# Optimization experiments

Measured on AMD Instinct MI355X. Metric: run time of the kernel, lower is better.

## Reference

```python
import jax, jax.numpy as jnp
import numpy as np

VOCAB, HID, L, HEADS, INTER, MAXSEQ, NCLS = 30522, 128, 2, 2, 512, 512, 2
HEAD = HID // HEADS
B, S = 128, 512


def _tlin(x, W, b):
    # TernaryLinear: threshold-quantize W to {-1,0,1} with per-tensor scale,
    # then ordinary linear. delta = 0.7*mean|W|, alpha = mean|W| over kept entries.
    absW = jnp.abs(W)
    delta = 0.7 * jnp.mean(absW)
    mask = (absW > delta).astype(W.dtype)
    alpha = jnp.sum(absW * mask) / jnp.maximum(jnp.sum(mask), 1.0)
    Wq = jnp.sign(W) * mask * alpha  # [out, in]
    return jnp.einsum('...i,oi->...o', x, Wq) + b


def _ln(x, g, b, eps=1e-5):
    m = jnp.mean(x, axis=-1, keepdims=True)
    v = jnp.var(x, axis=-1, keepdims=True)
    return (x - m) * jax.lax.rsqrt(v + eps) * g + b


def setup_inputs() -> dict:
    key = jax.random.key(0)
    ks = iter(jax.random.split(key, 64))
    n = lambda shape, s=0.02: jax.random.normal(next(ks), shape, dtype=jnp.float32) * s
    inp = {
        'input_ids': jax.random.randint(next(ks), (B, S), 0, VOCAB, dtype=jnp.int32).astype(jnp.int64),
        'tok_emb': n((VOCAB, HID)),
        'pos_emb': n((MAXSEQ, HID)),
        'ln_g': jnp.ones((HID,), jnp.float32), 'ln_b': jnp.zeros((HID,), jnp.float32),
        'qw': n((L, HID, HID)), 'qb': jnp.zeros((L, HID), jnp.float32),
        'kw': n((L, HID, HID)), 'kb': jnp.zeros((L, HID), jnp.float32),
        'vw': n((L, HID, HID)), 'vb': jnp.zeros((L, HID), jnp.float32),
        'aow': n((L, HID, HID)), 'aob': jnp.zeros((L, HID), jnp.float32),
        'iw': n((L, INTER, HID)), 'ib': jnp.zeros((L, INTER), jnp.float32),
        'fow': n((L, HID, INTER)), 'fob': jnp.zeros((L, HID), jnp.float32),
        'ln1g': jnp.ones((L, HID), jnp.float32), 'ln1b': jnp.zeros((L, HID), jnp.float32),
        'ln2g': jnp.ones((L, HID), jnp.float32), 'ln2b': jnp.zeros((L, HID), jnp.float32),
        'clf_w': n((NCLS, HID)), 'clf_b': jnp.zeros((NCLS,), jnp.float32),
    }
    return inp


def reference(input_ids, tok_emb, pos_emb, ln_g, ln_b, qw, qb, kw, kb, vw, vb,
              aow, aob, iw, ib, fow, fob, ln1g, ln1b, ln2g, ln2b, clf_w, clf_b):
    b, s = input_ids.shape
    x = tok_emb[input_ids] + pos_emb[jnp.arange(s)][None, :, :]  # [B,S,H]
    x = _ln(x, ln_g, ln_b)
    scale = 1.0 / (HEAD ** 0.5)
    for l in range(L):
        q = _tlin(x, qw[l], qb[l]).reshape(b, s, HEADS, HEAD)
        k = _tlin(x, kw[l], kb[l]).reshape(b, s, HEADS, HEAD)
        v = _tlin(x, vw[l], vb[l]).reshape(b, s, HEADS, HEAD)
        scores = jnp.einsum('bqhd,bkhd->bhqk', q, k) * scale
        attn = jax.nn.softmax(scores, axis=-1)
        ctx = jnp.einsum('bhqk,bkhd->bqhd', attn, v).reshape(b, s, HID)
        attn_out = _tlin(ctx, aow[l], aob[l])
        x = _ln(x + attn_out, ln1g[l], ln1b[l])
        ff = _tlin(jax.nn.relu(_tlin(x, iw[l], ib[l])), fow[l], fob[l])
        x = _ln(x + ff, ln2g[l], ln2b[l])
    cls = x[:, 0, :]
    logits = _tlin(cls, clf_w, clf_b)  # [B, NCLS]
    return logits
```

## Files before the change

### kernel.cpp

```cpp
#include <hip/hip_runtime.h>

typedef short bf8s __attribute__((ext_vector_type(8)));
typedef float f32x4 __attribute__((ext_vector_type(4)));

#define MFMA16(a, b, c) __builtin_amdgcn_mfma_f32_16x16x32_bf16(a, b, c, 0, 0, 0)

constexpr int S_ = 512, HID_ = 128, B_ = 128, M_ = B_ * S_;

__device__ inline short f2bf(float f) {
  unsigned u = __float_as_uint(f);
  u = (u + 0x7fffu + ((u >> 16) & 1u)) >> 16;
  return (short)u;
}
__device__ inline float bf2f(short s) {
  return __uint_as_float(((unsigned)(unsigned short)s) << 16);
}

__device__ inline float block_red1024(float v, float* red) {
  #pragma unroll
  for (int m = 32; m >= 1; m >>= 1) v += __shfl_xor(v, m);
  __syncthreads();
  if ((threadIdx.x & 63) == 0) red[threadIdx.x >> 6] = v;
  __syncthreads();
  float t = 0.f;
  #pragma unroll
  for (int i = 0; i < 16; ++i) t += red[i];
  return t;
}

__device__ inline void mat_info(int mat, const float* qw, const float* kw,
                                const float* vw, const float* aow, const float* iw,
                                const float* fw, const float* cw,
                                const float** src, int* n, int* doff) {
  if (mat < 6) {
    int l = mat / 3, which = mat % 3;
    const float* t[3] = {qw, kw, vw};
    *src = t[which] + l * 16384; *n = 16384; *doff = l * 49152 + which * 16384;
  } else if (mat < 8) {
    int l = mat - 6;
    *src = aow + l * 16384; *n = 16384; *doff = 98304 + l * 16384;
  } else if (mat < 10) {
    *src = iw + (mat - 8) * 65536; *n = 65536; *doff = 131072 + (mat - 8) * 65536;
  } else if (mat < 12) {
    *src = fw + (mat - 10) * 65536; *n = 65536; *doff = 262144 + (mat - 10) * 65536;
  } else {
    *src = cw; *n = 256; *doff = 393216;
  }
}

__global__ __launch_bounds__(1024) void k_qe(const float* qw, const float* kw,
    const float* vw, const float* aow, const float* iw, const float* fw,
    const float* cw, short* WQ,
    const int* __restrict__ ids, const float* __restrict__ tok,
    const float* __restrict__ pos, const float* __restrict__ g,
    const float* __restrict__ bb, short* xb) {
  __shared__ float red[16];
  int tid = threadIdx.x;
  if (blockIdx.x < 13) {
    const float* src; int n, doff;
    mat_info(blockIdx.x, qw, kw, vw, aow, iw, fw, cw, &src, &n, &doff);
    float s = 0.f;
    for (int i = tid; i < n; i += 1024) s += fabsf(src[i]);
    s = block_red1024(s, red);
    float delta = 0.7f * s / (float)n;
    float s2 = 0.f, c2 = 0.f;
    for (int i = tid; i < n; i += 1024) {
      float a = fabsf(src[i]);
      if (a > delta) { s2 += a; c2 += 1.f; }
    }
    s2 = block_red1024(s2, red);
    c2 = block_red1024(c2, red);
    float alpha = s2 / fmaxf(c2, 1.f);
    for (int i = tid; i < n; i += 1024) {
      float w = src[i];
      WQ[doff + i] = (fabsf(w) > delta) ? f2bf(w > 0.f ? alpha : -alpha) : (short)0;
    }
  } else {
    int wave = tid >> 6, lane = tid & 63;
    int t = (blockIdx.x - 13) * 16 + wave;
    int s = t & (S_ - 1);
    int id = ids[t];
    float e0 = tok[(size_t)id * HID_ + lane] + pos[(size_t)s * HID_ + lane];
    float e1 = tok[(size_t)id * HID_ + 64 + lane] + pos[(size_t)s * HID_ + 64 + lane];
    float sum = e0 + e1, ssq = e0 * e0 + e1 * e1;
    #pragma unroll
    for (int m = 32; m >= 1; m >>= 1) {
      sum += __shfl_xor(sum, m);
      ssq += __shfl_xor(ssq, m);
    }
    float mean = sum / 128.f;
    float var = ssq / 128.f - mean * mean;
    float rs = rsqrtf(var + 1e-5f);
    size_t o = (size_t)t * HID_;
    xb[o + lane]      = f2bf((e0 - mean) * rs * g[lane] + bb[lane]);
    xb[o + 64 + lane] = f2bf((e1 - mean) * rs * g[64 + lane] + bb[64 + lane]);
  }
}

__global__ __launch_bounds__(256) void k_qkv(
    const short* __restrict__ A, const short* __restrict__ W,
    const float* __restrict__ b0, const float* __restrict__ b1,
    const float* __restrict__ b2, short* outb) {
  __shared__ short Wl[128 * 144];
  int tid = threadIdx.x, lane = tid & 63, wave = tid >> 6;
  int row16 = lane & 15, quad = lane >> 4;
  int tok0 = blockIdx.x * 64 + wave * 16;
  int nbase = blockIdx.y * 128;

  const short* arow = A + (size_t)(tok0 + row16) * 128 + quad * 8;
  bf8s av[4];
  #pragma unroll
  for (int ki = 0; ki < 4; ++ki) av[ki] = *(const bf8s*)(arow + ki * 32);

  {
    int r = tid >> 1, half = tid & 1;
    const short* src = W + (size_t)(nbase + r) * 128 + half * 64;
    short* dst = &Wl[r * 144 + half * 64];
    #pragma unroll
    for (int j = 0; j < 8; ++j)
      *(bf8s*)(dst + j * 8) = *(const bf8s*)(src + j * 8);
  }
  __syncthreads();

  f32x4 acc[8] = {};
  #pragma unroll
  for (int ki = 0; ki < 4; ++ki)
    #pragma unroll
    for (int ot = 0; ot < 8; ++ot) {
      bf8s b = *(const bf8s*)(&Wl[(ot * 16 + row16) * 144 + ki * 32 + quad * 8]);
      acc[ot] = MFMA16(av[ki], b, acc[ot]);
    }

  const float* bp = (blockIdx.y == 0) ? b0 : ((blockIdx.y == 1) ? b1 : b2);
  float osc = (blockIdx.y == 0) ? 0.125f : 1.0f;
  int m0 = tok0 + quad * 4;
  #pragma unroll
  for (int ot = 0; ot < 8; ++ot) {
    int col = ot * 16 + row16;
    float bi = bp[col];
    #pragma unroll
    for (int r = 0; r < 4; ++r) {
      float v = (acc[ot][r] + bi) * osc;
      outb[(size_t)(m0 + r) * 384 + nbase + col] = f2bf(v);
    }
  }
}

template <int DOQKV>
__global__ __launch_bounds__(512, 2) void k_aoff(
    const short* __restrict__ cb, const short* __restrict__ Wa,
    const float* __restrict__ aob, const float* __restrict__ ln1g,
    const float* __restrict__ ln1b, const short* __restrict__ Wi,
    const short* __restrict__ Wf, const float* __restrict__ ib,
    const float* __restrict__ fb, const float* __restrict__ ln2g,
    const float* __restrict__ ln2b, short* xb,
    const short* __restrict__ Wqkv2, const float* __restrict__ qb2,
    const float* __restrict__ kb2, const float* __restrict__ vb2,
    short* qkvout) {
  __shared__ short SM[29696];
  int tid = threadIdx.x, lane = tid & 63, wave = tid >> 6;
  int row16 = lane & 15, quad = lane >> 4;
  int tok0 = blockIdx.x * 128 + wave * 16;
  int m0 = tok0 + quad * 4;

  const short* arow = cb + (size_t)(tok0 + row16) * 128 + quad * 8;
  bf8s av[4];
  #pragma unroll
  for (int ki = 0; ki < 4; ++ki) av[ki] = *(const bf8s*)(arow + ki * 32);

  {
    int r = tid >> 2, q4 = tid & 3;
    const short* src = Wa + (size_t)r * 128 + q4 * 32;
    short* dst = &SM[r * 144 + q4 * 32];
    #pragma unroll
    for (int j = 0; j < 4; ++j)
      *(bf8s*)(dst + j * 8) = *(const bf8s*)(src + j * 8);
  }
  __syncthreads();

  f32x4 acc[8] = {};
  #pragma unroll
  for (int ki = 0; ki < 4; ++ki)
    #pragma unroll
    for (int ot = 0; ot < 8; ++ot) {
      bf8s b = *(const bf8s*)(&SM[(ot * 16 + row16) * 144 + ki * 32 + quad * 8]);
      acc[ot] = MFMA16(av[ki], b, acc[ot]);
    }

  {
    float sum[4] = {}, ssq[4] = {};
    #pragma unroll
    for (int ot = 0; ot < 8; ++ot) {
      int col = ot * 16 + row16;
      float bi = aob[col];
      #pragma unroll
      for (int r = 0; r < 4; ++r) {
        float v = acc[ot][r] + bi + bf2f(xb[(size_t)(m0 + r) * HID_ + col]);
        acc[ot][r] = v;
        sum[r] += v; ssq[r] += v * v;
      }
    }
    #pragma unroll
    for (int m = 1; m <= 8; m <<= 1)
      #pragma unroll
      for (int r = 0; r < 4; ++r) {
        sum[r] += __shfl_xor(sum[r], m);
        ssq[r] += __shfl_xor(ssq[r], m);
      }
    float mean[4], rstd[4];
    #pragma unroll
    for (int r = 0; r < 4; ++r) {
      mean[r] = sum[r] / 128.f;
      float var = ssq[r] / 128.f - mean[r] * mean[r];
      rstd[r] = rsqrtf(var + 1e-5f);
    }
    #pragma unroll
    for (int ot = 0; ot < 8; ++ot) {
      int col = ot * 16 + row16;
      float gg = ln1g[col], bb2 = ln1b[col];
      #pragma unroll
      for (int r = 0; r < 4; ++r)
        acc[ot][r] = (acc[ot][r] - mean[r]) * rstd[r] * gg + bb2;
    }
  }

  #pragma unroll
  for (int ot = 0; ot < 8; ++ot) {
    int col = ot * 16 + row16;
    #pragma unroll
    for (int r = 0; r < 4; ++r)
      xb[(size_t)(m0 + r) * HID_ + col] = f2bf(acc[ot][r]);
  }

  __syncthreads();
  {
    short* myX = &SM[wave * 2304];
    #pragma unroll
    for (int ot = 0; ot < 8; ++ot)
      #pragma unroll
      for (int r = 0; r < 4; ++r)
        myX[(quad * 4 + r) * 144 + ot * 16 + row16] = f2bf(acc[ot][r]);
    #pragma unroll
    for (int ki = 0; ki < 4; ++ki)
      av[ki] = *(const bf8s*)(myX + row16 * 144 + ki * 32 + quad * 8);
  }

  int rwi = tid >> 3, q8 = tid & 7;
  int rwf = tid >> 2, qf4 = tid & 3;
  short* SWi = SM;
  short* SWf = SM + 9216;
  short* mySt = SM + 19456 + wave * 1280;
  f32x4 acc2[8] = {};
  for (int c = 0; c < 8; ++c) {
    __syncthreads();
    {
      const short* ws1 = Wi + (size_t)(c * 64 + rwi) * HID_ + q8 * 16;
      const short* ws2 = Wf + (size_t)rwf * 512 + c * 64 + qf4 * 16;
      bf8s a0 = *(const bf8s*)(ws1);
      bf8s a1 = *(const bf8s*)(ws1 + 8);
      bf8s b0 = *(const bf8s*)(ws2);
      bf8s b1 = *(const bf8s*)(ws2 + 8);
      short* dwi = SWi + rwi * 144 + q8 * 16;
      short* dwf = SWf + rwf * 80 + qf4 * 16;
      *(bf8s*)(dwi) = a0; *(bf8s*)(dwi + 8) = a1;
      *(bf8s*)(dwf) = b0; *(bf8s*)(dwf + 8) = b1;
    }
    __syncthreads();

    #pragma unroll
    for (int ot = 0; ot < 4; ++ot) {
      f32x4 hacc = {};
      #pragma unroll
      for (int ki = 0; ki < 4; ++ki) {
        bf8s b = *(const bf8s*)(SWi + (ot * 16 + row16) * 144 + ki * 32 + quad * 8);
        hacc = MFMA16(av[ki], b, hacc);
      }
      float bi = ib[c * 64 + ot * 16 + row16];
      #pragma unroll
      for (int r = 0; r < 4; ++r)
        mySt[(quad * 4 + r) * 80 + ot * 16 + row16] =
            f2bf(fmaxf(hacc[r] + bi, 0.f));
    }
    bf8s ha0 = *(const bf8s*)(mySt + row16 * 80 + quad * 8);
    bf8s ha1 = *(const bf8s*)(mySt + row16 * 80 + 32 + quad * 8);
    #pragma unroll
    for (int ot = 0; ot < 8; ++ot) {
      bf8s bA = *(const bf8s*)(SWf + (ot * 16 + row16) * 80 + quad * 8);
      bf8s bB = *(const bf8s*)(SWf + (ot * 16 + row16) * 80 + 32 + quad * 8);
      acc2[ot] = MFMA16(ha0, bA, acc2[ot]);
      acc2[ot] = MFMA16(ha1, bB, acc2[ot]);
    }
  }

  {
    float sum[4] = {}, ssq[4] = {};
    #pragma unroll
    for (int ot = 0; ot < 8; ++ot) {
      int col = ot * 16 + row16;
      float bi = fb[col];
      #pragma unroll
      for (int r = 0; r < 4; ++r) {
        float v = acc2[ot][r] + bi + bf2f(xb[(size_t)(m0 + r) * HID_ + col]);
        acc2[ot][r] = v;
        sum[r] += v; ssq[r] += v * v;
      }
    }
    #pragma unroll
    for (int m = 1; m <= 8; m <<= 1)
      #pragma unroll
      for (int r = 0; r < 4; ++r) {
        sum[r] += __shfl_xor(sum[r], m);
        ssq[r] += __shfl_xor(ssq[r], m);
      }
    float mean[4], rstd[4];
    #pragma unroll
    for (int r = 0; r < 4; ++r) {
      mean[r] = sum[r] / 128.f;
      float var = ssq[r] / 128.f - mean[r] * mean[r];
      rstd[r] = rsqrtf(var + 1e-5f);
    }
    #pragma unroll
    for (int ot = 0; ot < 8; ++ot) {
      int col = ot * 16 + row16;
      float gg = ln2g[col], bb2 = ln2b[col];
      #pragma unroll
      for (int r = 0; r < 4; ++r) {
        float v = (acc2[ot][r] - mean[r]) * rstd[r] * gg + bb2;
        acc2[ot][r] = v;
        xb[(size_t)(m0 + r) * HID_ + col] = f2bf(v);
      }
    }
  }

  if (DOQKV) {
    __syncthreads();
    bf8s av2[4];
    {
      short* myX = &SM[wave * 2304];
      #pragma unroll
      for (int ot = 0; ot < 8; ++ot)
        #pragma unroll
        for (int r = 0; r < 4; ++r)
          myX[(quad * 4 + r) * 144 + ot * 16 + row16] = f2bf(acc2[ot][r]);
      #pragma unroll
      for (int ki = 0; ki < 4; ++ki)
        av2[ki] = *(const bf8s*)(myX + row16 * 144 + ki * 32 + quad * 8);
    }
    for (int c3 = 0; c3 < 3; ++c3) {
      __syncthreads();
      {
        int r = tid >> 2, q4 = tid & 3;
        const short* src = Wqkv2 + (size_t)(c3 * 128 + r) * 128 + q4 * 32;
        short* dst = &SM[r * 144 + q4 * 32];
        #pragma unroll
        for (int j = 0; j < 4; ++j)
          *(bf8s*)(dst + j * 8) = *(const bf8s*)(src + j * 8);
      }
      __syncthreads();
      f32x4 acc3[8] = {};
      #pragma unroll
      for (int ki = 0; ki < 4; ++ki)
        #pragma unroll
        for (int ot = 0; ot < 8; ++ot) {
          bf8s b = *(const bf8s*)(&SM[(ot * 16 + row16) * 144 + ki * 32 + quad * 8]);
          acc3[ot] = MFMA16(av2[ki], b, acc3[ot]);
        }
      const float* bp = (c3 == 0) ? qb2 : ((c3 == 1) ? kb2 : vb2);
      float osc = (c3 == 0) ? 0.125f : 1.0f;
      #pragma unroll
      for (int ot = 0; ot < 8; ++ot) {
        int col = ot * 16 + row16;
        float bi = bp[col];
        #pragma unroll
        for (int r = 0; r < 4; ++r) {
          float v = (acc3[ot][r] + bi) * osc;
          qkvout[(size_t)(m0 + r) * 384 + c3 * 128 + col] = f2bf(v);
        }
      }
    }
  }
}

__global__ __launch_bounds__(512) void k_attn(const short* __restrict__ qkv,
                                              short* __restrict__ O) {
  __shared__ short Kl[64 * 72];
  __shared__ short Vtl[64 * 72];
  __shared__ short Pl[8][16 * 72];

  int tid = threadIdx.x, lane = tid & 63, wave = tid >> 6;
  int row16 = lane & 15, quad = lane >> 4;
  int b = blockIdx.x >> 2, h = (blockIdx.x >> 1) & 1, qhalf = blockIdx.x & 1;
  const short* base  = qkv + (size_t)b * S_ * 384;
  const short* kbase = base + 128 + h * 64;
  const short* vbase = base + 256 + h * 64;
  int q0 = qhalf * 256 + wave * 32;

  bf8s qa[2][2];
  #pragma unroll
  for (int qf = 0; qf < 2; ++qf) {
    const short* qrow = base + h * 64 +
        (size_t)(q0 + qf * 16 + row16) * 384 + quad * 8;
    qa[qf][0] = *(const bf8s*)(qrow);
    qa[qf][1] = *(const bf8s*)(qrow + 32);
  }

  int krow = tid >> 3, dgk = tid & 7;
  int vkey = tid & 63, dgv = tid >> 6;
  const short* kptr = kbase + (size_t)krow * 384 + dgk * 8;
  const short* vptr = vbase + (size_t)vkey * 384 + dgv * 8;
  bf8s kst = *(const bf8s*)(kptr);
  bf8s vst = *(const bf8s*)(vptr);

  float li[2][4] = {};
  f32x4 oacc[2][4] = {};
  short* myP = &Pl[wave][0];

  for (int kt0 = 0; kt0 < S_; kt0 += 64) {
    if (kt0) __syncthreads();
    *(bf8s*)(&Kl[krow * 72 + dgk * 8]) = kst;
    #pragma unroll
    for (int j = 0; j < 8; ++j) Vtl[(dgv * 8 + j) * 72 + vkey] = vst[j];
    __syncthreads();
    if (kt0 + 64 < S_) {
      kst = *(const bf8s*)(kptr + (size_t)(kt0 + 64) * 384);
      vst = *(const bf8s*)(vptr + (size_t)(kt0 + 64) * 384);
    }

    f32x4 sc[2][4] = {};
    #pragma unroll
    for (int ks = 0; ks < 4; ++ks) {
      const short* kp = &Kl[(ks * 16 + row16) * 72 + quad * 8];
      bf8s k0 = *(const bf8s*)(kp);
      bf8s k1 = *(const bf8s*)(kp + 32);
      sc[0][ks] = MFMA16(qa[0][0], k0, sc[0][ks]);
      sc[0][ks] = MFMA16(qa[0][1], k1, sc[0][ks]);
      sc[1][ks] = MFMA16(qa[1][0], k0, sc[1][ks]);
      sc[1][ks] = MFMA16(qa[1][1], k1, sc[1][ks]);
    }

    #pragma unroll
    for (int qf = 0; qf < 2; ++qf) {
      #pragma unroll
      for (int ks = 0; ks < 4; ++ks)
        #pragma unroll
        for (int r = 0; r < 4; ++r) {
          float pv = __expf(sc[qf][ks][r]);
          li[qf][r] += pv;
          myP[(quad * 4 + r) * 72 + ks * 16 + row16] = f2bf(pv);
        }
      bf8s pa0 = *(const bf8s*)(&myP[row16 * 72 + quad * 8]);
      bf8s pa1 = *(const bf8s*)(&myP[row16 * 72 + 32 + quad * 8]);
      #pragma unroll
      for (int dt = 0; dt < 4; ++dt) {
        const short* vp = &Vtl[(dt * 16 + row16) * 72 + quad * 8];
        bf8s v0 = *(const bf8s*)(vp);
        bf8s v1 = *(const bf8s*)(vp + 32);
        oacc[qf][dt] = MFMA16(pa0, v0, oacc[qf][dt]);
        oacc[qf][dt] = MFMA16(pa1, v1, oacc[qf][dt]);
      }
    }
  }

  #pragma unroll
  for (int qf = 0; qf < 2; ++qf) {
    float inv[4];
    #pragma unroll
    for (int r = 0; r < 4; ++r) {
      float t = li[qf][r];
      #pragma unroll
      for (int m = 1; m <= 8; m <<= 1) t += __shfl_xor(t, m);
      inv[r] = 1.f / t;
    }
    size_t trow = (size_t)(b * S_ + q0 + qf * 16 + quad * 4);
    #pragma unroll
    for (int dt = 0; dt < 4; ++dt)
      #pragma unroll
      for (int r = 0; r < 4; ++r)
        O[(trow + r) * HID_ + h * 64 + dt * 16 + row16] =
            f2bf(oacc[qf][dt][r] * inv[r]);
  }
}

__global__ __launch_bounds__(256) void k_clf(const short* __restrict__ xb,
    const short* __restrict__ Wc, const float* __restrict__ cbias, float* out) {
  int i = threadIdx.x;
  int b = i >> 1, c = i & 1;
  float s = 0.f;
  for (int k = 0; k < HID_; ++k)
    s += bf2f(xb[(size_t)b * S_ * HID_ + k]) * bf2f(Wc[c * HID_ + k]);
  out[b * 2 + c] = s + cbias[c];
}

extern "C" void kernel_launch(void* const* d_in, const int* in_sizes, int n_in,
                              void* d_out, int out_size, void* d_ws, size_t ws_size,
                              hipStream_t stream) {
  const int*   ids     = (const int*)d_in[0];
  const float* tok_emb = (const float*)d_in[1];
  const float* pos_emb = (const float*)d_in[2];
  const float* ln_g    = (const float*)d_in[3];
  const float* ln_bb   = (const float*)d_in[4];
  const float* qw      = (const float*)d_in[5];
  const float* qbias   = (const float*)d_in[6];
  const float* kw      = (const float*)d_in[7];
  const float* kbias   = (const float*)d_in[8];
  const float* vw      = (const float*)d_in[9];
  const float* vbias   = (const float*)d_in[10];
  const float* aow     = (const float*)d_in[11];
  const float* aobias  = (const float*)d_in[12];
  const float* iw      = (const float*)d_in[13];
  const float* ibias   = (const float*)d_in[14];
  const float* fow     = (const float*)d_in[15];
  const float* fbias   = (const float*)d_in[16];
  const float* ln1g    = (const float*)d_in[17];
  const float* ln1b    = (const float*)d_in[18];
  const float* ln2g    = (const float*)d_in[19];
  const float* ln2b    = (const float*)d_in[20];
  const float* clfw    = (const float*)d_in[21];
  const float* clfb    = (const float*)d_in[22];

  char* ws = (char*)d_ws;
  short* WQ  = (short*)ws;
  short* xb  = (short*)(ws + 1048576);
  short* qkv = (short*)(ws + 1048576 + 16777216);
  short* cb_ = qkv + (size_t)M_ * 384;

  k_qe<<<13 + M_ / 16, 1024, 0, stream>>>(qw, kw, vw, aow, iw, fow, clfw, WQ,
                                          ids, tok_emb, pos_emb, ln_g, ln_bb, xb);

  const short* Wqkv0 = WQ;
  const short* Wqkv1 = WQ + 49152;
  const short* Wa0   = WQ + 98304;
  const short* Wa1   = WQ + 98304 + 16384;
  const short* Wi0   = WQ + 131072;
  const short* Wi1   = WQ + 131072 + 65536;
  const short* Wf0   = WQ + 262144;
  const short* Wf1   = WQ + 262144 + 65536;

  k_qkv<<<dim3(M_ / 64, 3), 256, 0, stream>>>(
      xb, Wqkv0, qbias, kbias, vbias, qkv);
  k_attn<<<512, 512, 0, stream>>>(qkv, cb_);
  k_aoff<1><<<M_ / 128, 512, 0, stream>>>(
      cb_, Wa0, aobias, ln1g, ln1b, Wi0, Wf0, ibias, fbias, ln2g, ln2b, xb,
      Wqkv1, qbias + HID_, kbias + HID_, vbias + HID_, qkv);
  k_attn<<<512, 512, 0, stream>>>(qkv, cb_);
  k_aoff<0><<<M_ / 128, 512, 0, stream>>>(
      cb_, Wa1, aobias + HID_, ln1g + HID_, ln1b + HID_, Wi1, Wf1,
      ibias + 512, fbias + HID_, ln2g + HID_, ln2b + HID_, xb,
      nullptr, nullptr, nullptr, nullptr, nullptr);

  k_clf<<<1, 256, 0, stream>>>(xb, WQ + 393216, clfb, (float*)d_out);
}
```

Baseline: 320.0 us.

## Prefetch weight tiles into registers and keep residual in registers in aoff kernel

Register-prefetches the next Wi/Wf chunk and the QKV weight tiles while the current chunk computes, replacing load-then-store staging. Loads the residual early and keeps the LN1 output packed in registers instead of re-reading xb from global memory. Writes the final x through shared memory as coalesced 16-byte rows. Raises the launch-bounds occupancy hint to 4 blocks, which adds register pressure alongside the extra prefetch and residual registers and could cause spills.

Measured after the change: 325.3 us. Within noise of the previous version (+1.7%).

```diff
diff --git a/kernel.cpp b/kernel.cpp
--- a/kernel.cpp
+++ b/kernel.cpp
@@ -147,7 +147,7 @@
 }
 
 template <int DOQKV>
-__global__ __launch_bounds__(512, 2) void k_aoff(
+__global__ __launch_bounds__(512, 4) void k_aoff(
     const short* __restrict__ cb, const short* __restrict__ Wa,
     const float* __restrict__ aob, const float* __restrict__ ln1g,
     const float* __restrict__ ln1b, const short* __restrict__ Wi,
@@ -162,6 +162,8 @@
   int row16 = lane & 15, quad = lane >> 4;
   int tok0 = blockIdx.x * 128 + wave * 16;
   int m0 = tok0 + quad * 4;
+  int rs4 = tid >> 2, q4 = tid & 3;
+  int rwi = tid >> 3, q8 = tid & 7;
 
   const short* arow = cb + (size_t)(tok0 + row16) * 128 + quad * 8;
   bf8s av[4];
@@ -169,13 +171,21 @@
   for (int ki = 0; ki < 4; ++ki) av[ki] = *(const bf8s*)(arow + ki * 32);
 
   {
-    int r = tid >> 2, q4 = tid & 3;
-    const short* src = Wa + (size_t)r * 128 + q4 * 32;
-    short* dst = &SM[r * 144 + q4 * 32];
+    const short* src = Wa + (size_t)rs4 * 128 + q4 * 32;
+    short* dst = &SM[rs4 * 144 + q4 * 32];
     #pragma unroll
     for (int j = 0; j < 4; ++j)
       *(bf8s*)(dst + j * 8) = *(const bf8s*)(src + j * 8);
   }
+
+  float resid[8][4];
+  #pragma unroll
+  for (int ot = 0; ot < 8; ++ot) {
+    int col = ot * 16 + row16;
+    #pragma unroll
+    for (int r = 0; r < 4; ++r)
+      resid[ot][r] = bf2f(xb[(size_t)(m0 + r) * HID_ + col]);
+  }
   __syncthreads();
 
   f32x4 acc[8] = {};
@@ -187,6 +197,14 @@
       acc[ot] = MFMA16(av[ki], b, acc[ot]);
     }
 
+  bf8s pf0, pf1, pf2, pf3;
+  {
+    const short* ws1 = Wi + (size_t)rwi * HID_ + q8 * 16;
+    const short* ws2 = Wf + (size_t)rs4 * 512 + q4 * 16;
+    pf0 = *(const bf8s*)(ws1); pf1 = *(const bf8s*)(ws1 + 8);
+    pf2 = *(const bf8s*)(ws2); pf3 = *(const bf8s*)(ws2 + 8);
+  }
+
   {
     float sum[4] = {}, ssq[4] = {};
     #pragma unroll
@@ -195,7 +213,7 @@
       float bi = aob[col];
       #pragma unroll
       for (int r = 0; r < 4; ++r) {
-        float v = acc[ot][r] + bi + bf2f(xb[(size_t)(m0 + r) * HID_ + col]);
+        float v = acc[ot][r] + bi + resid[ot][r];
         acc[ot][r] = v;
         sum[r] += v; ssq[r] += v * v;
       }
@@ -224,29 +242,31 @@
     }
   }
 
+  unsigned xp[16];
   #pragma unroll
   for (int ot = 0; ot < 8; ++ot) {
-    int col = ot * 16 + row16;
-    #pragma unroll
-    for (int r = 0; r < 4; ++r)
-      xb[(size_t)(m0 + r) * HID_ + col] = f2bf(acc[ot][r]);
+    xp[2 * ot] = (unsigned)(unsigned short)f2bf(acc[ot][0]) |
+                 ((unsigned)(unsigned short)f2bf(acc[ot][1]) << 16);
+    xp[2 * ot + 1] = (unsigned)(unsigned short)f2bf(acc[ot][2]) |
+                     ((unsigned)(unsigned short)f2bf(acc[ot][3]) << 16);
   }
 
   __syncthreads();
-  {
-    short* myX = &SM[wave * 2304];
-    #pragma unroll
-    for (int ot = 0; ot < 8; ++ot)
-      #pragma unroll
-      for (int r = 0; r < 4; ++r)
-        myX[(quad * 4 + r) * 144 + ot * 16 + row16] = f2bf(acc[ot][r]);
+  short* myX = &SM[wave * 2304];
+  {
+    #pragma unroll
+    for (int ot = 0; ot < 8; ++ot) {
+      int col = ot * 16 + row16;
+      myX[(quad * 4 + 0) * 144 + col] = (short)(xp[2 * ot] & 0xffffu);
+      myX[(quad * 4 + 1) * 144 + col] = (short)(xp[2 * ot] >> 16);
+      myX[(quad * 4 + 2) * 144 + col] = (short)(xp[2 * ot + 1] & 0xffffu);
+      myX[(quad * 4 + 3) * 144 + col] = (short)(xp[2 * ot + 1] >> 16);
+    }
     #pragma unroll
     for (int ki = 0; ki < 4; ++ki)
       av[ki] = *(const bf8s*)(myX + row16 * 144 + ki * 32 + quad * 8);
   }
 
-  int rwi = tid >> 3, q8 = tid & 7;
-  int rwf = tid >> 2, qf4 = tid & 3;
   short* SWi = SM;
   short* SWf = SM + 9216;
   short* mySt = SM + 19456 + wave * 1280;
@@ -254,18 +274,22 @@
   for (int c = 0; c < 8; ++c) {
     __syncthreads();
     {
-      const short* ws1 = Wi + (size_t)(c * 64 + rwi) * HID_ + q8 * 16;
-      const short* ws2 = Wf + (size_t)rwf * 512 + c * 64 + qf4 * 16;
-      bf8s a0 = *(const bf8s*)(ws1);
-      bf8s a1 = *(const bf8s*)(ws1 + 8);
-      bf8s b0 = *(const bf8s*)(ws2);
-      bf8s b1 = *(const bf8s*)(ws2 + 8);
       short* dwi = SWi + rwi * 144 + q8 * 16;
-      short* dwf = SWf + rwf * 80 + qf4 * 16;
-      *(bf8s*)(dwi) = a0; *(bf8s*)(dwi + 8) = a1;
-      *(bf8s*)(dwf) = b0; *(bf8s*)(dwf + 8) = b1;
+      short* dwf = SWf + rs4 * 80 + q4 * 16;
+      *(bf8s*)(dwi) = pf0; *(bf8s*)(dwi + 8) = pf1;
+      *(bf8s*)(dwf) = pf2; *(bf8s*)(dwf + 8) = pf3;
     }
     __syncthreads();
+    if (c < 7) {
+      const short* ws1 = Wi + (size_t)((c + 1) * 64 + rwi) * HID_ + q8 * 16;
+      const short* ws2 = Wf + (size_t)rs4 * 512 + (c + 1) * 64 + q4 * 16;
+      pf0 = *(const bf8s*)(ws1); pf1 = *(const bf8s*)(ws1 + 8);
+      pf2 = *(const bf8s*)(ws2); pf3 = *(const bf8s*)(ws2 + 8);
+    } else if (DOQKV) {
+      const short* src = Wqkv2 + (size_t)rs4 * 128 + q4 * 32;
+      pf0 = *(const bf8s*)(src);      pf1 = *(const bf8s*)(src + 8);
+      pf2 = *(const bf8s*)(src + 16); pf3 = *(const bf8s*)(src + 24);
+    }
 
     #pragma unroll
     for (int ot = 0; ot < 4; ++ot) {
@@ -300,7 +324,10 @@
       float bi = fb[col];
       #pragma unroll
       for (int r = 0; r < 4; ++r) {
-        float v = acc2[ot][r] + bi + bf2f(xb[(size_t)(m0 + r) * HID_ + col]);
+        unsigned u = xp[2 * ot + (r >> 1)];
+        float xv = (r & 1) ? __uint_as_float(u & 0xffff0000u)
+                           : __uint_as_float(u << 16);
+        float v = acc2[ot][r] + bi + xv;
         acc2[ot][r] = v;
         sum[r] += v; ssq[r] += v * v;
       }
@@ -324,39 +351,45 @@
       int col = ot * 16 + row16;
       float gg = ln2g[col], bb2 = ln2b[col];
       #pragma unroll
-      for (int r = 0; r < 4; ++r) {
-        float v = (acc2[ot][r] - mean[r]) * rstd[r] * gg + bb2;
-        acc2[ot][r] = v;
-        xb[(size_t)(m0 + r) * HID_ + col] = f2bf(v);
-      }
-    }
+      for (int r = 0; r < 4; ++r)
+        acc2[ot][r] = (acc2[ot][r] - mean[r]) * rstd[r] * gg + bb2;
+    }
+  }
+
+  __syncthreads();
+  #pragma unroll
+  for (int ot = 0; ot < 8; ++ot) {
+    int col = ot * 16 + row16;
+    #pragma unroll
+    for (int r = 0; r < 4; ++r)
+      myX[(quad * 4 + r) * 144 + col] = f2bf(acc2[ot][r]);
+  }
+  {
+    int xr = lane >> 2, xs = (lane & 3) * 32;
+    short* xrow = xb + (size_t)(tok0 + xr) * HID_ + xs;
+    #pragma unroll
+    for (int j = 0; j < 4; ++j)
+      *(bf8s*)(xrow + j * 8) = *(const bf8s*)(myX + xr * 144 + xs + j * 8);
   }
 
   if (DOQKV) {
-    __syncthreads();
     bf8s av2[4];
-    {
-      short* myX = &SM[wave * 2304];
-      #pragma unroll
-      for (int ot = 0; ot < 8; ++ot)
-        #pragma unroll
-        for (int r = 0; r < 4; ++r)
-          myX[(quad * 4 + r) * 144 + ot * 16 + row16] = f2bf(acc2[ot][r]);
-      #pragma unroll
-      for (int ki = 0; ki < 4; ++ki)
-        av2[ki] = *(const bf8s*)(myX + row16 * 144 + ki * 32 + quad * 8);
-    }
+    #pragma unroll
+    for (int ki = 0; ki < 4; ++ki)
+      av2[ki] = *(const bf8s*)(myX + row16 * 144 + ki * 32 + quad * 8);
     for (int c3 = 0; c3 < 3; ++c3) {
       __syncthreads();
       {
-        int r = tid >> 2, q4 = tid & 3;
-        const short* src = Wqkv2 + (size_t)(c3 * 128 + r) * 128 + q4 * 32;
-        short* dst = &SM[r * 144 + q4 * 32];
-        #pragma unroll
-        for (int j = 0; j < 4; ++j)
-          *(bf8s*)(dst + j * 8) = *(const bf8s*)(src + j * 8);
+        short* dst = &SM[rs4 * 144 + q4 * 32];
+        *(bf8s*)(dst) = pf0;      *(bf8s*)(dst + 8) = pf1;
+        *(bf8s*)(dst + 16) = pf2; *(bf8s*)(dst + 24) = pf3;
       }
       __syncthreads();
+      if (c3 < 2) {
+        const short* src = Wqkv2 + (size_t)((c3 + 1) * 128 + rs4) * 128 + q4 * 32;
+        pf0 = *(const bf8s*)(src);      pf1 = *(const bf8s*)(src + 8);
+        pf2 = *(const bf8s*)(src + 16); pf3 = *(const bf8s*)(src + 24);
+      }
       f32x4 acc3[8] = {};
       #pragma unroll
       for (int ki = 0; ki < 4; ++ki)
```

## Read fused-layer weights directly from global memory and drop block barriers

Applied to the files above, without the earlier changes.

Restructures the fused attention-output/FFN kernel so that each wave reads weight fragments straight from global memory (L1/L2-cached) instead of staging them cooperatively in LDS with __syncthreads. Blocks shrink to 256 threads with a small per-wave LDS tile. That tile is used to stage the residual input and to write activations and qkv outputs as coalesced 16-byte rows instead of scattered 2-byte stores. The aim is to remove barrier stalls and LDS capacity limits on occupancy. The cost is more global/L2 weight traffic per wave, since the weights are no longer shared across waves through LDS.

After: 601.6 us. +88.0%, slower.

```diff
diff --git a/kernel.cpp b/kernel.cpp
--- a/kernel.cpp
+++ b/kernel.cpp
@@ -147,7 +147,7 @@
 }
 
 template <int DOQKV>
-__global__ __launch_bounds__(512, 2) void k_aoff(
+__global__ __launch_bounds__(256) void k_aoff(
     const short* __restrict__ cb, const short* __restrict__ Wa,
     const float* __restrict__ aob, const float* __restrict__ ln1g,
     const float* __restrict__ ln1b, const short* __restrict__ Wi,
@@ -157,33 +157,36 @@
     const short* __restrict__ Wqkv2, const float* __restrict__ qb2,
     const float* __restrict__ kb2, const float* __restrict__ vb2,
     short* qkvout) {
-  __shared__ short SM[29696];
+  __shared__ short SM[4 * 2304];
   int tid = threadIdx.x, lane = tid & 63, wave = tid >> 6;
   int row16 = lane & 15, quad = lane >> 4;
-  int tok0 = blockIdx.x * 128 + wave * 16;
+  int tok0 = blockIdx.x * 64 + wave * 16;
   int m0 = tok0 + quad * 4;
+  short* myX = &SM[wave * 2304];
+  int xr = lane >> 2, xs = (lane & 3) * 32;
+
+  {
+    const short* src = xb + (size_t)(tok0 + xr) * HID_ + xs;
+    bf8s x0 = *(const bf8s*)(src);
+    bf8s x1 = *(const bf8s*)(src + 8);
+    bf8s x2 = *(const bf8s*)(src + 16);
+    bf8s x3 = *(const bf8s*)(src + 24);
+    short* dst = myX + xr * 144 + xs;
+    *(bf8s*)(dst) = x0;      *(bf8s*)(dst + 8) = x1;
+    *(bf8s*)(dst + 16) = x2; *(bf8s*)(dst + 24) = x3;
+  }
 
   const short* arow = cb + (size_t)(tok0 + row16) * 128 + quad * 8;
   bf8s av[4];
   #pragma unroll
   for (int ki = 0; ki < 4; ++ki) av[ki] = *(const bf8s*)(arow + ki * 32);
 
-  {
-    int r = tid >> 2, q4 = tid & 3;
-    const short* src = Wa + (size_t)r * 128 + q4 * 32;
-    short* dst = &SM[r * 144 + q4 * 32];
-    #pragma unroll
-    for (int j = 0; j < 4; ++j)
-      *(bf8s*)(dst + j * 8) = *(const bf8s*)(src + j * 8);
-  }
-  __syncthreads();
-
   f32x4 acc[8] = {};
   #pragma unroll
   for (int ki = 0; ki < 4; ++ki)
     #pragma unroll
     for (int ot = 0; ot < 8; ++ot) {
-      bf8s b = *(const bf8s*)(&SM[(ot * 16 + row16) * 144 + ki * 32 + quad * 8]);
+      bf8s b = *(const bf8s*)(Wa + (size_t)(ot * 16 + row16) * 128 + ki * 32 + quad * 8);
       acc[ot] = MFMA16(av[ki], b, acc[ot]);
     }
 
@@ -195,7 +198,7 @@
       float bi = aob[col];
       #pragma unroll
       for (int r = 0; r < 4; ++r) {
-        float v = acc[ot][r] + bi + bf2f(xb[(size_t)(m0 + r) * HID_ + col]);
+        float v = acc[ot][r] + bi + bf2f(myX[(quad * 4 + r) * 144 + col]);
         acc[ot][r] = v;
         sum[r] += v; ssq[r] += v * v;
       }
@@ -229,67 +232,62 @@
     int col = ot * 16 + row16;
     #pragma unroll
     for (int r = 0; r < 4; ++r)
-      xb[(size_t)(m0 + r) * HID_ + col] = f2bf(acc[ot][r]);
-  }
-
-  __syncthreads();
-  {
-    short* myX = &SM[wave * 2304];
-    #pragma unroll
-    for (int ot = 0; ot < 8; ++ot)
-      #pragma unroll
-      for (int r = 0; r < 4; ++r)
-        myX[(quad * 4 + r) * 144 + ot * 16 + row16] = f2bf(acc[ot][r]);
-    #pragma unroll
-    for (int ki = 0; ki < 4; ++ki)
-      av[ki] = *(const bf8s*)(myX + row16 * 144 + ki * 32 + quad * 8);
-  }
-
-  int rwi = tid >> 3, q8 = tid & 7;
-  int rwf = tid >> 2, qf4 = tid & 3;
-  short* SWi = SM;
-  short* SWf = SM + 9216;
-  short* mySt = SM + 19456 + wave * 1280;
+      myX[(quad * 4 + r) * 144 + col] = f2bf(acc[ot][r]);
+  }
+  #pragma unroll
+  for (int ki = 0; ki < 4; ++ki)
+    av[ki] = *(const bf8s*)(myX + row16 * 144 + ki * 32 + quad * 8);
+  {
+    const short* src = myX + xr * 144 + xs;
+    short* dst = xb + (size_t)(tok0 + xr) * HID_ + xs;
+    #pragma unroll
+    for (int j = 0; j < 4; ++j)
+      *(bf8s*)(dst + j * 8) = *(const bf8s*)(src + j * 8);
+  }
+
   f32x4 acc2[8] = {};
   for (int c = 0; c < 8; ++c) {
-    __syncthreads();
-    {
-      const short* ws1 = Wi + (size_t)(c * 64 + rwi) * HID_ + q8 * 16;
-      const short* ws2 = Wf + (size_t)rwf * 512 + c * 64 + qf4 * 16;
-      bf8s a0 = *(const bf8s*)(ws1);
-      bf8s a1 = *(const bf8s*)(ws1 + 8);
-      bf8s b0 = *(const bf8s*)(ws2);
-      bf8s b1 = *(const bf8s*)(ws2 + 8);
-      short* dwi = SWi + rwi * 144 + q8 * 16;
-      short* dwf = SWf + rwf * 80 + qf4 * 16;
-      *(bf8s*)(dwi) = a0; *(bf8s*)(dwi + 8) = a1;
-      *(bf8s*)(dwf) = b0; *(bf8s*)(dwf + 8) = b1;
-    }
-    __syncthreads();
-
     #pragma unroll
     for (int ot = 0; ot < 4; ++ot) {
       f32x4 hacc = {};
       #pragma unroll
       for (int ki = 0; ki < 4; ++ki) {
-        bf8s b = *(const bf8s*)(SWi + (ot * 16 + row16) * 144 + ki * 32 + quad * 8);
+        bf8s b = *(const bf8s*)(Wi + (size_t)(c * 64 + ot * 16 + row16) * 128 + ki * 32 + quad * 8);
         hacc = MFMA16(av[ki], b, hacc);
       }
       float bi = ib[c * 64 + ot * 16 + row16];
       #pragma unroll
       for (int r = 0; r < 4; ++r)
-        mySt[(quad * 4 + r) * 80 + ot * 16 + row16] =
+        myX[(quad * 4 + r) * 80 + ot * 16 + row16] =
             f2bf(fmaxf(hacc[r] + bi, 0.f));
     }
-    bf8s ha0 = *(const bf8s*)(mySt + row16 * 80 + quad * 8);
-    bf8s ha1 = *(const bf8s*)(mySt + row16 * 80 + 32 + quad * 8);
-    #pragma unroll
-    for (int ot = 0; ot < 8; ++ot) {
-      bf8s bA = *(const bf8s*)(SWf + (ot * 16 + row16) * 80 + quad * 8);
-      bf8s bB = *(const bf8s*)(SWf + (ot * 16 + row16) * 80 + 32 + quad * 8);
-      acc2[ot] = MFMA16(ha0, bA, acc2[ot]);
-      acc2[ot] = MFMA16(ha1, bB, acc2[ot]);
-    }
+    {
+      bf8s ha0 = *(const bf8s*)(myX + row16 * 80 + quad * 8);
+      #pragma unroll
+      for (int ot = 0; ot < 8; ++ot) {
+        bf8s bA = *(const bf8s*)(Wf + (size_t)(ot * 16 + row16) * 512 + c * 64 + quad * 8);
+        acc2[ot] = MFMA16(ha0, bA, acc2[ot]);
+      }
+    }
+    {
+      bf8s ha1 = *(const bf8s*)(myX + row16 * 80 + 32 + quad * 8);
+      #pragma unroll
+      for (int ot = 0; ot < 8; ++ot) {
+        bf8s bB = *(const bf8s*)(Wf + (size_t)(ot * 16 + row16) * 512 + c * 64 + 32 + quad * 8);
+        acc2[ot] = MFMA16(ha1, bB, acc2[ot]);
+      }
+    }
+  }
+
+  {
+    const short* src = xb + (size_t)(tok0 + xr) * HID_ + xs;
+    bf8s x0 = *(const bf8s*)(src);
+    bf8s x1 = *(const bf8s*)(src + 8);
+    bf8s x2 = *(const bf8s*)(src + 16);
+    bf8s x3 = *(const bf8s*)(src + 24);
+    short* dst = myX + xr * 144 + xs;
+    *(bf8s*)(dst) = x0;      *(bf8s*)(dst + 8) = x1;
+    *(bf8s*)(dst + 16) = x2; *(bf8s*)(dst + 24) = x3;
   }
 
   {
@@ -300,7 +298,7 @@
       float bi = fb[col];
       #pragma unroll
       for (int r = 0; r < 4; ++r) {
-        float v = acc2[ot][r] + bi + bf2f(xb[(size_t)(m0 + r) * HID_ + col]);
+        float v = acc2[ot][r] + bi + bf2f(myX[(quad * 4 + r) * 144 + col]);
         acc2[ot][r] = v;
         sum[r] += v; ssq[r] += v * v;
       }
@@ -324,45 +322,38 @@
       int col = ot * 16 + row16;
       float gg = ln2g[col], bb2 = ln2b[col];
       #pragma unroll
-      for (int r = 0; r < 4; ++r) {
-        float v = (acc2[ot][r] - mean[r]) * rstd[r] * gg + bb2;
-        acc2[ot][r] = v;
-        xb[(size_t)(m0 + r) * HID_ + col] = f2bf(v);
-      }
-    }
+      for (int r = 0; r < 4; ++r)
+        acc2[ot][r] = (acc2[ot][r] - mean[r]) * rstd[r] * gg + bb2;
+    }
+  }
+
+  #pragma unroll
+  for (int ot = 0; ot < 8; ++ot) {
+    int col = ot * 16 + row16;
+    #pragma unroll
+    for (int r = 0; r < 4; ++r)
+      myX[(quad * 4 + r) * 144 + col] = f2bf(acc2[ot][r]);
+  }
+  {
+    const short* src = myX + xr * 144 + xs;
+    short* dst = xb + (size_t)(tok0 + xr) * HID_ + xs;
+    #pragma unroll
+    for (int j = 0; j < 4; ++j)
+      *(bf8s*)(dst + j * 8) = *(const bf8s*)(src + j * 8);
   }
 
   if (DOQKV) {
-    __syncthreads();
     bf8s av2[4];
-    {
-      short* myX = &SM[wave * 2304];
-      #pragma unroll
-      for (int ot = 0; ot < 8; ++ot)
-        #pragma unroll
-        for (int r = 0; r < 4; ++r)
-          myX[(quad * 4 + r) * 144 + ot * 16 + row16] = f2bf(acc2[ot][r]);
-      #pragma unroll
-      for (int ki = 0; ki < 4; ++ki)
-        av2[ki] = *(const bf8s*)(myX + row16 * 144 + ki * 32 + quad * 8);
-    }
+    #pragma unroll
+    for (int ki = 0; ki < 4; ++ki)
+      av2[ki] = *(const bf8s*)(myX + row16 * 144 + ki * 32 + quad * 8);
     for (int c3 = 0; c3 < 3; ++c3) {
-      __syncthreads();
-      {
-        int r = tid >> 2, q4 = tid & 3;
-        const short* src = Wqkv2 + (size_t)(c3 * 128 + r) * 128 + q4 * 32;
-        short* dst = &SM[r * 144 + q4 * 32];
-        #pragma unroll
-        for (int j = 0; j < 4; ++j)
-          *(bf8s*)(dst + j * 8) = *(const bf8s*)(src + j * 8);
-      }
-      __syncthreads();
       f32x4 acc3[8] = {};
       #pragma unroll
       for (int ki = 0; ki < 4; ++ki)
         #pragma unroll
         for (int ot = 0; ot < 8; ++ot) {
-          bf8s b = *(const bf8s*)(&SM[(ot * 16 + row16) * 144 + ki * 32 + quad * 8]);
+          bf8s b = *(const bf8s*)(Wqkv2 + (size_t)(c3 * 128 + ot * 16 + row16) * 128 + ki * 32 + quad * 8);
           acc3[ot] = MFMA16(av2[ki], b, acc3[ot]);
         }
       const float* bp = (c3 == 0) ? qb2 : ((c3 == 1) ? kb2 : vb2);
@@ -372,10 +363,15 @@
         int col = ot * 16 + row16;
         float bi = bp[col];
         #pragma unroll
-        for (int r = 0; r < 4; ++r) {
-          float v = (acc3[ot][r] + bi) * osc;
-          qkvout[(size_t)(m0 + r) * 384 + c3 * 128 + col] = f2bf(v);
-        }
+        for (int r = 0; r < 4; ++r)
+          myX[(quad * 4 + r) * 144 + col] = f2bf((acc3[ot][r] + bi) * osc);
+      }
+      {
+        const short* src = myX + xr * 144 + xs;
+        short* dst = qkvout + (size_t)(tok0 + xr) * 384 + c3 * 128 + xs;
+        #pragma unroll
+        for (int j = 0; j < 4; ++j)
+          *(bf8s*)(dst + j * 8) = *(const bf8s*)(src + j * 8);
       }
     }
   }
@@ -539,11 +535,11 @@
   k_qkv<<<dim3(M_ / 64, 3), 256, 0, stream>>>(
       xb, Wqkv0, qbias, kbias, vbias, qkv);
   k_attn<<<512, 512, 0, stream>>>(qkv, cb_);
-  k_aoff<1><<<M_ / 128, 512, 0, stream>>>(
+  k_aoff<1><<<M_ / 64, 256, 0, stream>>>(
       cb_, Wa0, aobias, ln1g, ln1b, Wi0, Wf0, ibias, fbias, ln2g, ln2b, xb,
       Wqkv1, qbias + HID_, kbias + HID_, vbias + HID_, qkv);
   k_attn<<<512, 512, 0, stream>>>(qkv, cb_);
-  k_aoff<0><<<M_ / 128, 512, 0, stream>>>(
+  k_aoff<0><<<M_ / 64, 256, 0, stream>>>(
       cb_, Wa1, aobias + HID_, ln1g + HID_, ln1b + HID_, Wi1, Wf1,
       ibias + 512, fbias + HID_, ln2g + HID_, ln2b + HID_, xb,
       nullptr, nullptr, nullptr, nullptr, nullptr);
```
